# Kernel tuning notes

Hardware: AMD Instinct MI355X
Metric: run time of the kernel (lower is better)

Reference implementation:

```python
import jax, jax.numpy as jnp
import numpy as np

B, N, M = 64, 256, 16
ONF, OEF = 92, 41
NF, EF = 128, 64
FINAL = 128  # final_node_len; final_layer outputs FINAL//2


def _linear_params(key, fan_in, fan_out):
    # kaiming_uniform fan_in, relu: bound = sqrt(6/fan_in)
    bound = np.sqrt(6.0 / fan_in)
    W = jax.random.uniform(key, (fan_out, fan_in), jnp.float32, -bound, bound)
    b = jnp.zeros((fan_out,), jnp.float32)
    return W, b


def setup_inputs() -> dict:
    key = jax.random.key(0)
    ks = jax.random.split(key, 12)
    node_fea = jax.random.normal(ks[0], (B, N, ONF), jnp.float32)
    edge_fea = jax.random.normal(ks[1], (B, N, M, OEF), jnp.float32)
    edge_fea_idx = jax.random.randint(ks[2], (B, N, M), 0, N)
    dis = jax.random.uniform(ks[3], (N, N), jnp.float32)
    Wn, bn = _linear_params(ks[4], ONF, NF)
    We, be = _linear_params(ks[5], OEF, EF)
    W1, b1 = _linear_params(ks[6], 2 * NF + EF, 2 * NF)
    W2, b2 = _linear_params(ks[7], 2 * NF + EF, 2 * NF)
    W3, b3 = _linear_params(ks[8], 2 * NF + EF, 2 * NF)
    Wf, bf = _linear_params(ks[9], NF, FINAL // 2)
    return dict(node_fea=node_fea, edge_fea=edge_fea, edge_fea_idx=edge_fea_idx,
                dis=dis, Wn=Wn, bn=bn, We=We, be=be,
                W1=W1, b1=b1, a1=jnp.float32(0.7),
                W2=W2, b2=b2, a2=jnp.float32(0.7),
                W3=W3, b3=b3, a3=jnp.float32(0.7),
                Wf=Wf, bf=bf,
                DAw=jnp.float32(48.0 / 5.0), DAb=jnp.float32(-28.0 / 5.0))


def _conv(nf, ef, idx, W, b, alpha):
    # nf: [B,N,F]; ef: [B,N,M,E]; idx: [B,N,M]
    Bb, Nn, Mm = idx.shape
    F = nf.shape[-1]
    idx_c = jnp.maximum(idx, 0)
    gathered = jax.vmap(lambda x, i: x[i])(nf, idx_c)           # [B,N,M,F]
    self_exp = jnp.broadcast_to(nf[:, :, None, :], (Bb, Nn, Mm, F))
    total = jnp.concatenate([self_exp, gathered, ef], axis=-1)   # [B,N,M,2F+E]
    gated = jnp.einsum('bnmi,oi->bnmo', total, W) + b            # [B,N,M,2F]
    nbr_filter, nbr_core = jnp.split(gated, 2, axis=-1)
    mask = (idx >= 0).astype(nf.dtype)[..., None]
    nbr_filter = jax.nn.sigmoid(nbr_filter) * mask
    nbr_core = jax.nn.softplus(nbr_core)
    nbr_sumed = jnp.sum(nbr_filter * nbr_core, axis=2)           # [B,N,F]
    return jax.nn.softplus(alpha * nf + nbr_sumed)


def reference(node_fea, edge_fea, edge_fea_idx, dis,
              Wn, bn, We, be,
              W1, b1, a1, W2, b2, a2, W3, b3, a3,
              Wf, bf, DAw, DAb):
    nf = node_fea @ Wn.T + bn                                    # [B,N,NF]
    ef = edge_fea @ We.T + be                                    # [B,N,M,EF]
    nf = _conv(nf, ef, edge_fea_idx, W1, b1, a1)
    nf = _conv(nf, ef, edge_fea_idx, W2, b2, a2)
    nf = _conv(nf, ef, edge_fea_idx, W3, b3, a3)
    nf = nf @ Wf.T + bf                                          # [B,N,FINAL//2]
    DA = jax.nn.sigmoid(DAw * dis + DAb)                         # [N,N]
    node1 = jnp.einsum('ij,bjf->bif', DA, nf)
    return jnp.concatenate([nf, node1], axis=2)                  # [B,N,FINAL]
```

## Files before the change

### kernel.cpp

```cpp
#include <hip/hip_runtime.h>
#include <hip/hip_bf16.h>
#include <math.h>

#define Bb   64
#define Nn   256
#define Mm   16
#define ONF  92
#define OEF  41
#define NF   128
#define EF   64
#define KDIM 320
#define ODIM 256
#define FINAL 128
#define K0C  6

typedef __attribute__((ext_vector_type(8))) short short8;
typedef __attribute__((ext_vector_type(4))) float f32x4;

__device__ __forceinline__ float sigmoidf_(float x) {
    float e = __expf(-x);
    return __builtin_amdgcn_rcpf(1.0f + e);
}
__device__ __forceinline__ float softplusf_(float x) {
    return fmaxf(x, 0.0f) + __logf(1.0f + __expf(-fabsf(x)));
}
__device__ __forceinline__ __hip_bfloat16 to_bf16(float x) { return __float2bfloat16(x); }

__device__ __forceinline__ void swz(const float* __restrict__ in, __hip_bfloat16* __restrict__ out,
                                    int t, int Itot, int koff, int Kuse, int K0)
{
    int j = t & 7;
    int u = t >> 3;
    int lane = u & 63;
    int ln16 = lane & 15, q = lane >> 4;
    int v = u >> 6;
    int k0 = v % K0, tile = v / K0;
    int n = tile * 16 + ln16, k = k0 * 32 + q * 8 + j;
    out[t] = (k < Kuse) ? to_bf16(in[(size_t)n * Itot + koff + k]) : to_bf16(0.0f);
}

#define SZ_WET (OEF * EF)
#define SZ_WB  (16 * K0C * 512)
#define SZ_WS  (16 * 4 * 512)
#define SZ_WNB ((NF / 16) * 3 * 512)
#define SZ_WEB ((EF / 16) * 2 * 512)
#define SZ_WFB ((64 / 16) * 4 * 512)
#define SZ_DA  (Nn * Nn)
#define PREP_TOTAL (SZ_WET + 3 * SZ_WB + 3 * SZ_WS + SZ_WNB + SZ_WEB + SZ_WFB + SZ_DA)

__global__ __launch_bounds__(256) void k_prep(
    const float* __restrict__ We, const float* __restrict__ W1,
    const float* __restrict__ W2, const float* __restrict__ W3,
    const float* __restrict__ Wn, const float* __restrict__ Wf,
    const float* __restrict__ dis, const float* __restrict__ pw, const float* __restrict__ pb,
    float* __restrict__ WeT,
    __hip_bfloat16* __restrict__ W1b, __hip_bfloat16* __restrict__ W2b, __hip_bfloat16* __restrict__ W3b,
    __hip_bfloat16* __restrict__ W1s, __hip_bfloat16* __restrict__ W2s, __hip_bfloat16* __restrict__ W3s,
    __hip_bfloat16* __restrict__ Wnb, __hip_bfloat16* __restrict__ Web, __hip_bfloat16* __restrict__ Wfb,
    __hip_bfloat16* __restrict__ DAf)
{
    int t = blockIdx.x * 256 + threadIdx.x;
    if (t < SZ_WET) {
        int o = t / OEF, i = t - o * OEF;
        WeT[i * EF + o] = We[t];
        return;
    }
    t -= SZ_WET;
    if (t < SZ_WB) { swz(W1, W1b, t, KDIM, NF, 192, K0C); return; }
    t -= SZ_WB;
    if (t < SZ_WB) { swz(W2, W2b, t, KDIM, NF, 192, K0C); return; }
    t -= SZ_WB;
    if (t < SZ_WB) { swz(W3, W3b, t, KDIM, NF, 192, K0C); return; }
    t -= SZ_WB;
    if (t < SZ_WS) { swz(W1, W1s, t, KDIM, 0, NF, 4); return; }
    t -= SZ_WS;
    if (t < SZ_WS) { swz(W2, W2s, t, KDIM, 0, NF, 4); return; }
    t -= SZ_WS;
    if (t < SZ_WS) { swz(W3, W3s, t, KDIM, 0, NF, 4); return; }
    t -= SZ_WS;
    if (t < SZ_WNB) { swz(Wn, Wnb, t, ONF, 0, ONF, 3); return; }
    t -= SZ_WNB;
    if (t < SZ_WEB) { swz(We, Web, t, OEF, 0, OEF, 2); return; }
    t -= SZ_WEB;
    if (t < SZ_WFB) { swz(Wf, Wfb, t, NF, 0, NF, 4); return; }
    t -= SZ_WFB;
    if (t < SZ_DA) {
        int i = t >> 8, jx = t & 255;
        float v = sigmoidf_(fmaf(*pw, dis[t], *pb));
        int itile = i >> 4, ln16 = i & 15;
        int k0 = jx >> 5, q = (jx >> 3) & 3, jj = jx & 7;
        DAf[(size_t)((((itile * 8 + k0) << 6) + (q << 4) + ln16)) * 8 + jj] = to_bf16(v);
    }
}

template<int KIN, int K0, int NCOLS>
__device__ __forceinline__ void emb_body(
    int bid, const float* __restrict__ X, const __hip_bfloat16* __restrict__ Bswz,
    const float* __restrict__ bias, __hip_bfloat16* __restrict__ Y,
    __hip_bfloat16* A_s, __hip_bfloat16* O_s)
{
    constexpr int KP = K0 * 32;
    constexpr int TPW = NCOLS / 64;
    constexpr int OLD = NCOLS + 24;

    const int row0 = bid * 64;
    const int t = threadIdx.x;

    {
        const float4* Xb = (const float4*)(X + (size_t)row0 * KIN);
        constexpr int NV = (64 * KIN) / 4;
        for (int c = t; c < NV; c += 256) {
            float4 v = Xb[c];
            int flat = c * 4;
            #pragma unroll
            for (int e = 0; e < 4; e++) {
                int f = flat + e;
                int row = f / KIN, k = f - row * KIN;
                int mt = row >> 4, ln16 = row & 15;
                int k0 = k >> 5, q = (k >> 3) & 3, j = k & 7;
                float vv = (e == 0) ? v.x : (e == 1) ? v.y : (e == 2) ? v.z : v.w;
                A_s[(((mt * K0 + k0) << 6) + (q << 4) + ln16) * 8 + j] = to_bf16(vv);
            }
        }
        constexpr int PAD = KP - KIN;
        for (int c = t; c < 64 * PAD; c += 256) {
            int row = c / PAD, k = KIN + (c - row * PAD);
            int mt = row >> 4, ln16 = row & 15;
            int k0 = k >> 5, q = (k >> 3) & 3, j = k & 7;
            A_s[(((mt * K0 + k0) << 6) + (q << 4) + ln16) * 8 + j] = to_bf16(0.0f);
        }
    }
    __syncthreads();

    const int wv = t >> 6, lane = t & 63;
    const int q = lane >> 4, ln16 = lane & 15;

    f32x4 acc[4][TPW];
    #pragma unroll
    for (int p = 0; p < TPW; p++) {
        float bv = bias[(wv * TPW + p) * 16 + ln16];
        #pragma unroll
        for (int mt = 0; mt < 4; mt++) acc[mt][p] = (f32x4){bv, bv, bv, bv};
    }

    short8 bw[TPW][K0];
    #pragma unroll
    for (int p = 0; p < TPW; p++)
        #pragma unroll
        for (int k0 = 0; k0 < K0; k0++)
            bw[p][k0] = *(const short8*)(Bswz + ((size_t)((wv * TPW + p) * K0 + k0) << 9) + (lane << 3));

    #pragma unroll
    for (int k0 = 0; k0 < K0; k0++) {
        short8 af[4];
        #pragma unroll
        for (int mt = 0; mt < 4; mt++)
            af[mt] = *(const short8*)(A_s + (((mt * K0 + k0) << 6) + lane) * 8);
        #pragma unroll
        for (int mt = 0; mt < 4; mt++)
            #pragma unroll
            for (int p = 0; p < TPW; p++)
                acc[mt][p] = __builtin_amdgcn_mfma_f32_16x16x32_bf16(af[mt], bw[p][k0], acc[mt][p], 0, 0, 0);
    }

    #pragma unroll
    for (int mt = 0; mt < 4; mt++)
        #pragma unroll
        for (int p = 0; p < TPW; p++) {
            int col = (wv * TPW + p) * 16 + ln16;
            #pragma unroll
            for (int r = 0; r < 4; r++)
                O_s[(mt * 16 + q * 4 + r) * OLD + col] = to_bf16(acc[mt][p][r]);
        }
    __syncthreads();
    constexpr int CH = NCOLS / 8;
    for (int c = t; c < 64 * CH; c += 256) {
        int row = c / CH, ch = c - row * CH;
        *(uint4*)(Y + (size_t)(row0 + row) * NCOLS + ch * 8) =
            *(const uint4*)(O_s + row * OLD + ch * 8);
    }
}

__global__ __launch_bounds__(256) void k_embed_all(
    const float* __restrict__ node_fea, const __hip_bfloat16* __restrict__ Wnb,
    const float* __restrict__ bn, __hip_bfloat16* __restrict__ nf0,
    const float* __restrict__ edge_fea, const __hip_bfloat16* __restrict__ Web,
    const float* __restrict__ be, __hip_bfloat16* __restrict__ efb)
{
    __shared__ __align__(16) __hip_bfloat16 A_s[4 * 3 * 512];
    __shared__ __align__(16) __hip_bfloat16 O_s[64 * (NF + 24)];
    if (blockIdx.x < 256)
        emb_body<ONF, 3, NF>(blockIdx.x, node_fea, Wnb, bn, nf0, A_s, O_s);
    else
        emb_body<OEF, 2, EF>(blockIdx.x - 256, edge_fea, Web, be, efb, A_s, O_s);
}

template<bool PRECOMP>
__global__ __launch_bounds__(512, 4) void k_conv_mfma(
    const __hip_bfloat16* __restrict__ nf_in,
    const float* __restrict__ edge_fea,
    const __hip_bfloat16* __restrict__ ef_bf,
    const int*   __restrict__ eidx,
    const float* __restrict__ WeT,
    const float* __restrict__ be,
    const __hip_bfloat16* __restrict__ Wb,
    const __hip_bfloat16* __restrict__ Wsb,
    const float* __restrict__ bias,
    const float* __restrict__ palpha,
    __hip_bfloat16* __restrict__ nf_out)
{
    __shared__ __align__(16) __hip_bfloat16 A_s[4 * K0C * 512];
    __shared__ __align__(16) __hip_bfloat16 A_sf[4 * 512];

    const int node0 = blockIdx.x * 4;
    const int b = node0 >> 8;
    const int t = threadIdx.x;
    const int wv = t >> 6, lane = t & 63;
    const int q = lane >> 4, ln16 = lane & 15;

    const unsigned long long mball = __ballot(eidx[node0 * Mm + lane] >= 0);

    if (wv < 4) {
        const int v = wv;
        int j = eidx[(node0 + v) * Mm + ln16];
        j = j < 0 ? 0 : j;
        const __hip_bfloat16* gathp = nf_in + (size_t)((b << 8) + j) * NF;
        #pragma unroll
        for (int k0 = 0; k0 < 4; k0++)
            *(uint4*)(A_s + ((v * K0C + k0) * 64 + lane) * 8) =
                *(const uint4*)(gathp + k0 * 32 + q * 8);
    } else {
        const int v = wv - 4;
        if (PRECOMP) {
            if (lane < 32) {
                const int q2 = q;
                const __hip_bfloat16* efp = ef_bf + (size_t)((node0 << 4) + v * 16 + ln16) * EF;
                #pragma unroll
                for (int qq = 0; qq < 4; qq++)
                    *(uint4*)(A_s + ((v * K0C + 4 + q2) * 64 + qq * 16 + ln16) * 8) =
                        *(const uint4*)(efp + q2 * 32 + qq * 8);
            } else if (lane < 48) {
                const int c = ln16;
                *(uint4*)(A_sf + (((c >> 2) * 64) + (c & 3) * 16 + v) * 8) =
                    *(const uint4*)(nf_in + (size_t)(node0 + v) * NF + c * 8);
            }
        } else {
            if (lane >= 32 && lane < 48) {
                const int c = ln16;
                *(uint4*)(A_sf + (((c >> 2) * 64) + (c & 3) * 16 + v) * 8) =
                    *(const uint4*)(nf_in + (size_t)(node0 + v) * NF + c * 8);
            }
        }
    }
    if (!PRECOMP) {
        for (int c = t; c < 64 * EF; c += 512) {
            int rr = c >> 6, col = c & 63;
            float a = be[col];
            const float* er = edge_fea + (size_t)(node0 * Mm + rr) * OEF;
            #pragma unroll
            for (int i = 0; i < OEF; i++) a = fmaf(er[i], WeT[i * EF + col], a);
            int mt = rr >> 4, l16 = rr & 15;
            int k0 = 4 + (col >> 5), qq = (col >> 3) & 3, jj = col & 7;
            A_s[((mt * K0C + k0) * 64 + qq * 16 + l16) * 8 + jj] = to_bf16(a);
        }
    }
    __syncthreads();

    f32x4 sv0, sv1;
    {
        float bF = bias[wv * 16 + ln16], bC = bias[(wv + 8) * 16 + ln16];
        sv0 = (f32x4){bF, bF, bF, bF};
        sv1 = (f32x4){bC, bC, bC, bC};
    }
    #pragma unroll
    for (int k0 = 0; k0 < 4; k0++) {
        short8 afs = *(const short8*)(A_sf + (k0 * 64 + lane) * 8);
        short8 bws0 = *(const short8*)(Wsb + ((size_t)(wv * 4 + k0) << 9) + (lane << 3));
        short8 bws1 = *(const short8*)(Wsb + ((size_t)((wv + 8) * 4 + k0) << 9) + (lane << 3));
        sv0 = __builtin_amdgcn_mfma_f32_16x16x32_bf16(afs, bws0, sv0, 0, 0, 0);
        sv1 = __builtin_amdgcn_mfma_f32_16x16x32_bf16(afs, bws1, sv1, 0, 0, 0);
    }

    f32x4 accF[4], accC[4];
    #pragma unroll
    for (int mt = 0; mt < 4; mt++) {
        float vF = __shfl(sv0[mt], ln16);
        float vC = __shfl(sv1[mt], ln16);
        accF[mt] = (f32x4){vF, vF, vF, vF};
        accC[mt] = (f32x4){vC, vC, vC, vC};
    }

    const __hip_bfloat16* WF = Wb + ((size_t)wv * (K0C * 512)) + (lane << 3);
    const __hip_bfloat16* WC = Wb + ((size_t)(wv + 8) * (K0C * 512)) + (lane << 3);
    short8 bwF[K0C], bwC[K0C];
    #pragma unroll
    for (int k0 = 0; k0 < K0C; k0++) {
        bwF[k0] = *(const short8*)(WF + k0 * 512);
        bwC[k0] = *(const short8*)(WC + k0 * 512);
    }

    #pragma unroll
    for (int k0 = 0; k0 < K0C; k0++) {
        short8 af[4];
        #pragma unroll
        for (int mt = 0; mt < 4; mt++)
            af[mt] = *(const short8*)(A_s + ((mt * K0C + k0) * 64 + lane) * 8);
        #pragma unroll
        for (int mt = 0; mt < 4; mt++) {
            accF[mt] = __builtin_amdgcn_mfma_f32_16x16x32_bf16(af[mt], bwF[k0], accF[mt], 0, 0, 0);
            accC[mt] = __builtin_amdgcn_mfma_f32_16x16x32_bf16(af[mt], bwC[k0], accC[mt], 0, 0, 0);
        }
    }

    const float alpha = *palpha;
    #pragma unroll
    for (int mt = 0; mt < 4; mt++) {
        const int gnode = node0 + mt;
        float partial = 0.0f;
        #pragma unroll
        for (int r = 0; r < 4; r++) {
            bool msk = (mball >> (mt * 16 + q * 4 + r)) & 1ull;
            float f = sigmoidf_(accF[mt][r]);
            float c = softplusf_(accC[mt][r]);
            partial += msk ? f * c : 0.0f;
        }
        partial += __shfl_xor(partial, 16);
        partial += __shfl_xor(partial, 32);
        if (q == 0) {
            int col = wv * 16 + ln16;
            float self = __bfloat162float(nf_in[(size_t)gnode * NF + col]);
            nf_out[(size_t)gnode * NF + col] = to_bf16(softplusf_(fmaf(alpha, self, partial)));
        }
    }
}

__global__ __launch_bounds__(256) void k_final_mfma(
    const __hip_bfloat16* __restrict__ nf, const __hip_bfloat16* __restrict__ Wfb,
    const float* __restrict__ bfv, float* __restrict__ out,
    __hip_bfloat16* __restrict__ XT)
{
    __shared__ __align__(16) __hip_bfloat16 A_s[16 * 512];
    const int node0 = blockIdx.x * 64;
    const int bloc = node0 >> 8;
    const int t = threadIdx.x;
    const int wv = t >> 6, lane = t & 63;
    const int q = lane >> 4, ln16 = lane & 15;

    const __hip_bfloat16* rowp = nf + (size_t)(node0 + (wv << 4) + ln16) * NF;
    #pragma unroll
    for (int k0 = 0; k0 < 4; k0++)
        *(uint4*)(A_s + ((wv * 4 + k0) * 64 + lane) * 8) =
            *(const uint4*)(rowp + k0 * 32 + q * 8);
    __syncthreads();

    short8 bw[4];
    #pragma unroll
    for (int k0 = 0; k0 < 4; k0++)
        bw[k0] = *(const short8*)(Wfb + ((size_t)(wv * 4 + k0) * 64 + lane) * 8);

    float bv = bfv[wv * 16 + ln16];
    f32x4 acc[4];
    #pragma unroll
    for (int mt = 0; mt < 4; mt++) acc[mt] = (f32x4){bv, bv, bv, bv};

    #pragma unroll
    for (int k0 = 0; k0 < 4; k0++) {
        short8 af[4];
        #pragma unroll
        for (int mt = 0; mt < 4; mt++)
            af[mt] = *(const short8*)(A_s + ((mt * 4 + k0) * 64 + lane) * 8);
        #pragma unroll
        for (int mt = 0; mt < 4; mt++)
            acc[mt] = __builtin_amdgcn_mfma_f32_16x16x32_bf16(af[mt], bw[k0], acc[mt], 0, 0, 0);
    }

    const int col = (wv << 4) + ln16;
    #pragma unroll
    for (int mt = 0; mt < 4; mt++)
        #pragma unroll
        for (int r = 0; r < 4; r++) {
            int row = mt * 16 + q * 4 + r;
            float v = acc[mt][r];
            out[(size_t)(node0 + row) * FINAL + col] = v;
            XT[(size_t)(bloc * 64 + col) * 256 + (node0 & 255) + row] = to_bf16(v);
        }
}

__global__ __launch_bounds__(256) void k_node1_mfma(
    const __hip_bfloat16* __restrict__ DAf,
    const __hip_bfloat16* __restrict__ XT,
    float* __restrict__ out)
{
    __shared__ __align__(16) __hip_bfloat16 B_s[32 * 512];
    const int blk = blockIdx.x;
    const int b = blk >> 2, i0 = (blk & 3) * 64;
    const int t = threadIdx.x;
    const int wv = t >> 6, lane = t & 63;
    const int q = lane >> 4, ln16 = lane & 15;

    const __hip_bfloat16* xrow = XT + (size_t)(b * 64 + (wv << 4) + ln16) * 256;
    #pragma unroll
    for (int k0 = 0; k0 < 8; k0++)
        *(uint4*)(B_s + ((wv * 8 + k0) * 64 + lane) * 8) =
            *(const uint4*)(xrow + k0 * 32 + q * 8);
    __syncthreads();

    f32x4 acc[4];
    #pragma unroll
    for (int mt = 0; mt < 4; mt++) acc[mt] = (f32x4){0.f, 0.f, 0.f, 0.f};

    #pragma unroll
    for (int k0 = 0; k0 < 8; k0++) {
        short8 bfr = *(const short8*)(B_s + ((wv * 8 + k0) * 64 + lane) * 8);
        short8 af[4];
        #pragma unroll
        for (int mt = 0; mt < 4; mt++)
            af[mt] = *(const short8*)(DAf + (size_t)(((i0 >> 4) + mt) * 8 + k0) * 512 + (lane << 3));
        #pragma unroll
        for (int mt = 0; mt < 4; mt++)
            acc[mt] = __builtin_amdgcn_mfma_f32_16x16x32_bf16(af[mt], bfr, acc[mt], 0, 0, 0);
    }

    #pragma unroll
    for (int mt = 0; mt < 4; mt++)
        #pragma unroll
        for (int r = 0; r < 4; r++) {
            int i = i0 + mt * 16 + q * 4 + r;
            out[(size_t)((b << 8) + i) * FINAL + 64 + (wv << 4) + ln16] = acc[mt][r];
        }
}

extern "C" void kernel_launch(void* const* d_in, const int* in_sizes, int n_in,
                              void* d_out, int out_size, void* d_ws, size_t ws_size,
                              hipStream_t stream)
{
    const float* node_fea = (const float*)d_in[0];
    const float* edge_fea = (const float*)d_in[1];
    const int*   eidx     = (const int*)  d_in[2];
    const float* dis      = (const float*)d_in[3];
    const float* Wn = (const float*)d_in[4];
    const float* bn = (const float*)d_in[5];
    const float* We = (const float*)d_in[6];
    const float* be = (const float*)d_in[7];
    const float* W1 = (const float*)d_in[8];
    const float* b1 = (const float*)d_in[9];
    const float* a1 = (const float*)d_in[10];
    const float* W2 = (const float*)d_in[11];
    const float* b2 = (const float*)d_in[12];
    const float* a2 = (const float*)d_in[13];
    const float* W3 = (const float*)d_in[14];
    const float* b3 = (const float*)d_in[15];
    const float* a3 = (const float*)d_in[16];
    const float* Wf = (const float*)d_in[17];
    const float* bf = (const float*)d_in[18];
    const float* DAw = (const float*)d_in[19];
    const float* DAb = (const float*)d_in[20];
    float* out = (float*)d_out;

    char* base = (char*)d_ws;
    size_t off = 0;
    auto alloc = [&](size_t bytes) { char* p = base + off; off = (off + bytes + 255) & ~(size_t)255; return p; };
    __hip_bfloat16* nfA = (__hip_bfloat16*)alloc((size_t)Bb * Nn * NF * 2);
    __hip_bfloat16* nfB = (__hip_bfloat16*)alloc((size_t)Bb * Nn * NF * 2);
    __hip_bfloat16* W1b = (__hip_bfloat16*)alloc((size_t)SZ_WB * 2);
    __hip_bfloat16* W2b = (__hip_bfloat16*)alloc((size_t)SZ_WB * 2);
    __hip_bfloat16* W3b = (__hip_bfloat16*)alloc((size_t)SZ_WB * 2);
    __hip_bfloat16* W1s = (__hip_bfloat16*)alloc((size_t)SZ_WS * 2);
    __hip_bfloat16* W2s = (__hip_bfloat16*)alloc((size_t)SZ_WS * 2);
    __hip_bfloat16* W3s = (__hip_bfloat16*)alloc((size_t)SZ_WS * 2);
    float* WeT = (float*)alloc((size_t)OEF * EF * 4);
    __hip_bfloat16* DAf = (__hip_bfloat16*)alloc((size_t)Nn * Nn * 2);
    __hip_bfloat16* Wnb = (__hip_bfloat16*)alloc((size_t)SZ_WNB * 2);
    __hip_bfloat16* Web = (__hip_bfloat16*)alloc((size_t)SZ_WEB * 2);
    __hip_bfloat16* Wfb = (__hip_bfloat16*)alloc((size_t)SZ_WFB * 2);
    __hip_bfloat16* XT  = (__hip_bfloat16*)alloc((size_t)Bb * 64 * Nn * 2);
    __hip_bfloat16* efb = (__hip_bfloat16*)alloc((size_t)Bb * Nn * Mm * EF * 2);
    const bool precomp = (ws_size >= off);

    hipLaunchKernelGGL(k_prep, dim3((PREP_TOTAL + 255) / 256), dim3(256), 0, stream,
                       We, W1, W2, W3, Wn, Wf, dis, DAw, DAb,
                       WeT, W1b, W2b, W3b, W1s, W2s, W3s, Wnb, Web, Wfb, DAf);

    hipLaunchKernelGGL(k_embed_all, dim3(precomp ? (256 + Bb * Nn * Mm / 64) : 256), dim3(256), 0, stream,
                       node_fea, Wnb, bn, nfA, edge_fea, Web, be, efb);

    if (precomp) {
        hipLaunchKernelGGL((k_conv_mfma<true>), dim3(Bb * Nn / 4), dim3(512), 0, stream,
                           nfA, edge_fea, efb, eidx, WeT, be, W1b, W1s, b1, a1, nfB);
        hipLaunchKernelGGL((k_conv_mfma<true>), dim3(Bb * Nn / 4), dim3(512), 0, stream,
                           nfB, edge_fea, efb, eidx, WeT, be, W2b, W2s, b2, a2, nfA);
        hipLaunchKernelGGL((k_conv_mfma<true>), dim3(Bb * Nn / 4), dim3(512), 0, stream,
                           nfA, edge_fea, efb, eidx, WeT, be, W3b, W3s, b3, a3, nfB);
    } else {
        hipLaunchKernelGGL((k_conv_mfma<false>), dim3(Bb * Nn / 4), dim3(512), 0, stream,
                           nfA, edge_fea, efb, eidx, WeT, be, W1b, W1s, b1, a1, nfB);
        hipLaunchKernelGGL((k_conv_mfma<false>), dim3(Bb * Nn / 4), dim3(512), 0, stream,
                           nfB, edge_fea, efb, eidx, WeT, be, W2b, W2s, b2, a2, nfA);
        hipLaunchKernelGGL((k_conv_mfma<false>), dim3(Bb * Nn / 4), dim3(512), 0, stream,
                           nfA, edge_fea, efb, eidx, WeT, be, W3b, W3s, b3, a3, nfB);
    }

    hipLaunchKernelGGL(k_final_mfma, dim3(Bb * Nn / 64), dim3(256), 0, stream, nfB, Wfb, bf, out, XT);
    hipLaunchKernelGGL(k_node1_mfma, dim3(Bb * 4), dim3(256), 0, stream, DAf, XT, out);
}
```

Measured before the change: 314.8 us.

## Process four node groups per conv block with register-prefetched software pipeline

Each conv block now handles 16 nodes in four groups of 4 instead of one group. The global loads (neighbor gathers, edge features, self features) for the next group are issued into registers while the current group's MFMAs run, then written to LDS after a barrier. The intent is to hide gather latency and amortize block launch and setup costs. In exchange the grid has a quarter as many blocks, and the per-group weights are reloaded from global/cache inside each compute step rather than held in registers. Extra barriers per group are also added.

```diff
diff --git a/kernel.cpp b/kernel.cpp
--- a/kernel.cpp
+++ b/kernel.cpp
@@ -212,125 +212,147 @@
     __shared__ __align__(16) __hip_bfloat16 A_s[4 * K0C * 512];
     __shared__ __align__(16) __hip_bfloat16 A_sf[4 * 512];
 
-    const int node0 = blockIdx.x * 4;
-    const int b = node0 >> 8;
+    const int node00 = blockIdx.x * 16;
+    const int b = node00 >> 8;
     const int t = threadIdx.x;
     const int wv = t >> 6, lane = t & 63;
     const int q = lane >> 4, ln16 = lane & 15;
-
-    const unsigned long long mball = __ballot(eidx[node0 * Mm + lane] >= 0);
-
-    if (wv < 4) {
-        const int v = wv;
-        int j = eidx[(node0 + v) * Mm + ln16];
-        j = j < 0 ? 0 : j;
-        const __hip_bfloat16* gathp = nf_in + (size_t)((b << 8) + j) * NF;
-        #pragma unroll
-        for (int k0 = 0; k0 < 4; k0++)
-            *(uint4*)(A_s + ((v * K0C + k0) * 64 + lane) * 8) =
-                *(const uint4*)(gathp + k0 * 32 + q * 8);
-    } else {
-        const int v = wv - 4;
-        if (PRECOMP) {
-            if (lane < 32) {
-                const int q2 = q;
-                const __hip_bfloat16* efp = ef_bf + (size_t)((node0 << 4) + v * 16 + ln16) * EF;
+    const int v4 = wv & 3;
+    const float alpha = *palpha;
+
+    int ej[4];
+    unsigned long long mb[4];
+    #pragma unroll
+    for (int g = 0; g < 4; g++) {
+        int node0 = node00 + g * 4;
+        mb[g] = __ballot(eidx[node0 * Mm + lane] >= 0);
+        int j = eidx[(node0 + v4) * Mm + ln16];
+        ej[g] = j < 0 ? 0 : j;
+    }
+
+    uint4 G0, G1, G2, G3, E0, E1, S;
+
+    auto load_regs = [&](int g) {
+        const int node0 = node00 + g * 4;
+        if (wv < 4) {
+            const __hip_bfloat16* gp = nf_in + (size_t)((b << 8) + ej[g]) * NF + q * 8;
+            G0 = *(const uint4*)(gp);
+            G1 = *(const uint4*)(gp + 32);
+            G2 = *(const uint4*)(gp + 64);
+            G3 = *(const uint4*)(gp + 96);
+        } else {
+            if (PRECOMP) {
+                const __hip_bfloat16* ep =
+                    ef_bf + ((size_t)(node0 * Mm) + v4 * 16 + ln16) * EF + q * 8;
+                E0 = *(const uint4*)(ep);
+                E1 = *(const uint4*)(ep + 32);
+            }
+            S = *(const uint4*)(nf_in + (size_t)(node0 + (ln16 & 3)) * NF + v4 * 32 + q * 8);
+        }
+    };
+
+    auto write_lds = [&](int g) {
+        if (wv < 4) {
+            *(uint4*)(A_s + ((wv * K0C + 0) * 64 + lane) * 8) = G0;
+            *(uint4*)(A_s + ((wv * K0C + 1) * 64 + lane) * 8) = G1;
+            *(uint4*)(A_s + ((wv * K0C + 2) * 64 + lane) * 8) = G2;
+            *(uint4*)(A_s + ((wv * K0C + 3) * 64 + lane) * 8) = G3;
+        } else {
+            if (PRECOMP) {
+                *(uint4*)(A_s + ((v4 * K0C + 4) * 64 + lane) * 8) = E0;
+                *(uint4*)(A_s + ((v4 * K0C + 5) * 64 + lane) * 8) = E1;
+            }
+            *(uint4*)(A_sf + (v4 * 64 + lane) * 8) = S;
+        }
+        if (!PRECOMP) {
+            const int node0 = node00 + g * 4;
+            for (int c = t; c < 64 * EF; c += 512) {
+                int rr = c >> 6, col = c & 63;
+                float a = be[col];
+                const float* er = edge_fea + (size_t)(node0 * Mm + rr) * OEF;
                 #pragma unroll
-                for (int qq = 0; qq < 4; qq++)
-                    *(uint4*)(A_s + ((v * K0C + 4 + q2) * 64 + qq * 16 + ln16) * 8) =
-                        *(const uint4*)(efp + q2 * 32 + qq * 8);
-            } else if (lane < 48) {
-                const int c = ln16;
-                *(uint4*)(A_sf + (((c >> 2) * 64) + (c & 3) * 16 + v) * 8) =
-                    *(const uint4*)(nf_in + (size_t)(node0 + v) * NF + c * 8);
-            }
-        } else {
-            if (lane >= 32 && lane < 48) {
-                const int c = ln16;
-                *(uint4*)(A_sf + (((c >> 2) * 64) + (c & 3) * 16 + v) * 8) =
-                    *(const uint4*)(nf_in + (size_t)(node0 + v) * NF + c * 8);
-            }
-        }
-    }
-    if (!PRECOMP) {
-        for (int c = t; c < 64 * EF; c += 512) {
-            int rr = c >> 6, col = c & 63;
-            float a = be[col];
-            const float* er = edge_fea + (size_t)(node0 * Mm + rr) * OEF;
+                for (int i = 0; i < OEF; i++) a = fmaf(er[i], WeT[i * EF + col], a);
+                int mt = rr >> 4, l16 = rr & 15;
+                int k0 = 4 + (col >> 5), qq = (col >> 3) & 3, jj = col & 7;
+                A_s[((mt * K0C + k0) * 64 + qq * 16 + l16) * 8 + jj] = to_bf16(a);
+            }
+        }
+    };
+
+    auto compute = [&](int g) {
+        const int node0 = node00 + g * 4;
+
+        f32x4 sv0, sv1;
+        {
+            float bF = bias[wv * 16 + ln16], bC = bias[(wv + 8) * 16 + ln16];
+            sv0 = (f32x4){bF, bF, bF, bF};
+            sv1 = (f32x4){bC, bC, bC, bC};
+        }
+        #pragma unroll
+        for (int k0 = 0; k0 < 4; k0++) {
+            short8 afs = *(const short8*)(A_sf + (k0 * 64 + lane) * 8);
+            short8 bws0 = *(const short8*)(Wsb + ((size_t)(wv * 4 + k0) << 9) + (lane << 3));
+            short8 bws1 = *(const short8*)(Wsb + ((size_t)((wv + 8) * 4 + k0) << 9) + (lane << 3));
+            sv0 = __builtin_amdgcn_mfma_f32_16x16x32_bf16(afs, bws0, sv0, 0, 0, 0);
+            sv1 = __builtin_amdgcn_mfma_f32_16x16x32_bf16(afs, bws1, sv1, 0, 0, 0);
+        }
+
+        f32x4 accF[4], accC[4];
+        #pragma unroll
+        for (int mt = 0; mt < 4; mt++) {
+            float vF = __shfl(sv0[mt], ln16);
+            float vC = __shfl(sv1[mt], ln16);
+            accF[mt] = (f32x4){vF, vF, vF, vF};
+            accC[mt] = (f32x4){vC, vC, vC, vC};
+        }
+
+        const __hip_bfloat16* WF = Wb + (size_t)wv * (K0C * 512) + (lane << 3);
+        const __hip_bfloat16* WC = Wb + (size_t)(wv + 8) * (K0C * 512) + (lane << 3);
+        #pragma unroll
+        for (int k0 = 0; k0 < K0C; k0++) {
+            short8 bwF = *(const short8*)(WF + k0 * 512);
+            short8 bwC = *(const short8*)(WC + k0 * 512);
+            short8 af[4];
             #pragma unroll
-            for (int i = 0; i < OEF; i++) a = fmaf(er[i], WeT[i * EF + col], a);
-            int mt = rr >> 4, l16 = rr & 15;
-            int k0 = 4 + (col >> 5), qq = (col >> 3) & 3, jj = col & 7;
-            A_s[((mt * K0C + k0) * 64 + qq * 16 + l16) * 8 + jj] = to_bf16(a);
-        }
-    }
-    __syncthreads();
-
-    f32x4 sv0, sv1;
-    {
-        float bF = bias[wv * 16 + ln16], bC = bias[(wv + 8) * 16 + ln16];
-        sv0 = (f32x4){bF, bF, bF, bF};
-        sv1 = (f32x4){bC, bC, bC, bC};
-    }
-    #pragma unroll
-    for (int k0 = 0; k0 < 4; k0++) {
-        short8 afs = *(const short8*)(A_sf + (k0 * 64 + lane) * 8);
-        short8 bws0 = *(const short8*)(Wsb + ((size_t)(wv * 4 + k0) << 9) + (lane << 3));
-        short8 bws1 = *(const short8*)(Wsb + ((size_t)((wv + 8) * 4 + k0) << 9) + (lane << 3));
-        sv0 = __builtin_amdgcn_mfma_f32_16x16x32_bf16(afs, bws0, sv0, 0, 0, 0);
-        sv1 = __builtin_amdgcn_mfma_f32_16x16x32_bf16(afs, bws1, sv1, 0, 0, 0);
-    }
-
-    f32x4 accF[4], accC[4];
-    #pragma unroll
-    for (int mt = 0; mt < 4; mt++) {
-        float vF = __shfl(sv0[mt], ln16);
-        float vC = __shfl(sv1[mt], ln16);
-        accF[mt] = (f32x4){vF, vF, vF, vF};
-        accC[mt] = (f32x4){vC, vC, vC, vC};
-    }
-
-    const __hip_bfloat16* WF = Wb + ((size_t)wv * (K0C * 512)) + (lane << 3);
-    const __hip_bfloat16* WC = Wb + ((size_t)(wv + 8) * (K0C * 512)) + (lane << 3);
-    short8 bwF[K0C], bwC[K0C];
-    #pragma unroll
-    for (int k0 = 0; k0 < K0C; k0++) {
-        bwF[k0] = *(const short8*)(WF + k0 * 512);
-        bwC[k0] = *(const short8*)(WC + k0 * 512);
-    }
-
-    #pragma unroll
-    for (int k0 = 0; k0 < K0C; k0++) {
-        short8 af[4];
-        #pragma unroll
-        for (int mt = 0; mt < 4; mt++)
-            af[mt] = *(const short8*)(A_s + ((mt * K0C + k0) * 64 + lane) * 8);
+            for (int mt = 0; mt < 4; mt++)
+                af[mt] = *(const short8*)(A_s + ((mt * K0C + k0) * 64 + lane) * 8);
+            #pragma unroll
+            for (int mt = 0; mt < 4; mt++) {
+                accF[mt] = __builtin_amdgcn_mfma_f32_16x16x32_bf16(af[mt], bwF, accF[mt], 0, 0, 0);
+                accC[mt] = __builtin_amdgcn_mfma_f32_16x16x32_bf16(af[mt], bwC, accC[mt], 0, 0, 0);
+            }
+        }
+
         #pragma unroll
         for (int mt = 0; mt < 4; mt++) {
-            accF[mt] = __builtin_amdgcn_mfma_f32_16x16x32_bf16(af[mt], bwF[k0], accF[mt], 0, 0, 0);
-            accC[mt] = __builtin_amdgcn_mfma_f32_16x16x32_bf16(af[mt], bwC[k0], accC[mt], 0, 0, 0);
-        }
-    }
-
-    const float alpha = *palpha;
-    #pragma unroll
-    for (int mt = 0; mt < 4; mt++) {
-        const int gnode = node0 + mt;
-        float partial = 0.0f;
-        #pragma unroll
-        for (int r = 0; r < 4; r++) {
-            bool msk = (mball >> (mt * 16 + q * 4 + r)) & 1ull;
-            float f = sigmoidf_(accF[mt][r]);
-            float c = softplusf_(accC[mt][r]);
-            partial += msk ? f * c : 0.0f;
-        }
-        partial += __shfl_xor(partial, 16);
-        partial += __shfl_xor(partial, 32);
-        if (q == 0) {
-            int col = wv * 16 + ln16;
-            float self = __bfloat162float(nf_in[(size_t)gnode * NF + col]);
-            nf_out[(size_t)gnode * NF + col] = to_bf16(softplusf_(fmaf(alpha, self, partial)));
-        }
+            const int gnode = node0 + mt;
+            unsigned mbits = (unsigned)(mb[g] >> (mt * 16 + q * 4)) & 0xFu;
+            float partial = 0.0f;
+            #pragma unroll
+            for (int r = 0; r < 4; r++) {
+                bool msk = (mbits >> r) & 1u;
+                float f = sigmoidf_(accF[mt][r]);
+                float c = softplusf_(accC[mt][r]);
+                partial += msk ? f * c : 0.0f;
+            }
+            partial += __shfl_xor(partial, 16);
+            partial += __shfl_xor(partial, 32);
+            if (q == 0) {
+                int col = wv * 16 + ln16;
+                float self = __bfloat162float(nf_in[(size_t)gnode * NF + col]);
+                nf_out[(size_t)gnode * NF + col] = to_bf16(softplusf_(fmaf(alpha, self, partial)));
+            }
+        }
+    };
+
+    load_regs(0);
+    #pragma unroll
+    for (int g = 0; g < 4; g++) {
+        if (g > 0) __syncthreads();
+        write_lds(g);
+        __syncthreads();
+        if (g < 3) load_regs(g + 1);
+        compute(g);
     }
 }
 
@@ -484,19 +506,20 @@
     hipLaunchKernelGGL(k_embed_all, dim3(precomp ? (256 + Bb * Nn * Mm / 64) : 256), dim3(256), 0, stream,
                        node_fea, Wnb, bn, nfA, edge_fea, Web, be, efb);
 
+    const int NBC = Bb * Nn / 16;
     if (precomp) {
-        hipLaunchKernelGGL((k_conv_mfma<true>), dim3(Bb * Nn / 4), dim3(512), 0, stream,
+        hipLaunchKernelGGL((k_conv_mfma<true>), dim3(NBC), dim3(512), 0, stream,
                            nfA, edge_fea, efb, eidx, WeT, be, W1b, W1s, b1, a1, nfB);
-        hipLaunchKernelGGL((k_conv_mfma<true>), dim3(Bb * Nn / 4), dim3(512), 0, stream,
+        hipLaunchKernelGGL((k_conv_mfma<true>), dim3(NBC), dim3(512), 0, stream,
                            nfB, edge_fea, efb, eidx, WeT, be, W2b, W2s, b2, a2, nfA);
-        hipLaunchKernelGGL((k_conv_mfma<true>), dim3(Bb * Nn / 4), dim3(512), 0, stream,
+        hipLaunchKernelGGL((k_conv_mfma<true>), dim3(NBC), dim3(512), 0, stream,
                            nfA, edge_fea, efb, eidx, WeT, be, W3b, W3s, b3, a3, nfB);
     } else {
-        hipLaunchKernelGGL((k_conv_mfma<false>), dim3(Bb * Nn / 4), dim3(512), 0, stream,
+        hipLaunchKernelGGL((k_conv_mfma<false>), dim3(NBC), dim3(512), 0, stream,
                            nfA, edge_fea, efb, eidx, WeT, be, W1b, W1s, b1, a1, nfB);
-        hipLaunchKernelGGL((k_conv_mfma<false>), dim3(Bb * Nn / 4), dim3(512), 0, stream,
+        hipLaunchKernelGGL((k_conv_mfma<false>), dim3(NBC), dim3(512), 0, stream,
                            nfB, edge_fea, efb, eidx, WeT, be, W2b, W2s, b2, a2, nfA);
-        hipLaunchKernelGGL((k_conv_mfma<false>), dim3(Bb * Nn / 4), dim3(512), 0, stream,
+        hipLaunchKernelGGL((k_conv_mfma<false>), dim3(NBC), dim3(512), 0, stream,
                            nfA, edge_fea, efb, eidx, WeT, be, W3b, W3s, b3, a3, nfB);
     }
 
```

New measurement: 379.1 us. 1.2x slower.
